# Kernel optimization log

Measured on AMD Instinct MI355X. Metric: run time of the kernel, lower is better.

Reference implementation:

```python
import math
import jax, jax.numpy as jnp
import numpy as np

D_MODEL = 1024
D_FF = 4096
NUM_EXPERTS = 8
TOP_K = 2
CAP_FACTOR = 1.0
AUX_COEF = 0.01
Z_COEF = 0.0


def setup_inputs() -> dict:
    key = jax.random.key(0)
    ks = jax.random.split(key, 6)
    x = jax.random.normal(ks[0], (4, 2048, D_MODEL), dtype=jnp.float32)
    router_w = jax.random.normal(ks[1], (D_MODEL, NUM_EXPERTS), dtype=jnp.float32) / math.sqrt(D_MODEL)
    router_b = jnp.zeros((NUM_EXPERTS,), dtype=jnp.float32)
    w1 = jax.random.normal(ks[2], (NUM_EXPERTS, D_MODEL, D_FF), dtype=jnp.float32) / math.sqrt(D_MODEL)
    w3 = jax.random.normal(ks[3], (NUM_EXPERTS, D_MODEL, D_FF), dtype=jnp.float32) / math.sqrt(D_MODEL)
    w2 = jax.random.normal(ks[4], (NUM_EXPERTS, D_FF, D_MODEL), dtype=jnp.float32) / math.sqrt(D_FF)
    return {"x": x, "router_w": router_w, "router_b": router_b, "w1": w1, "w3": w3, "w2": w2}


def reference(x, router_w, router_b, w1, w3, w2):
    b, s, d = x.shape
    E, k = NUM_EXPERTS, TOP_K
    T = b * s
    x_flat = x.reshape(T, d)

    # ---- router ----
    logits = x_flat @ router_w + router_b                      # [T, E]
    logits_f32 = logits.astype(jnp.float32)
    probs = jax.nn.softmax(logits_f32, axis=-1)                # [T, E]
    topk_p, topk_i = jax.lax.top_k(probs, k)                   # [T, k]
    topk_p = topk_p / jnp.clip(topk_p.sum(-1, keepdims=True), 1e-9)  # normalize_gates
    gate = topk_p.reshape(-1)                                  # [T*k]
    expert_idx = topk_i.reshape(-1)                            # [T*k]

    # ---- aux loss (load balance + z-loss) ----
    importance = probs.mean(axis=0)                            # [E]
    load = jnp.bincount(topk_i[:, 0], length=E).astype(jnp.float32) / T
    lb_loss = (importance * load).sum() * float(E)
    z_loss = jnp.mean(jnp.square(jax.nn.logsumexp(logits_f32, axis=-1)))
    aux_loss = (AUX_COEF * lb_loss + Z_COEF * z_loss).astype(x.dtype)

    # ---- capacity-based dispatch ----
    N = T * k
    cap = max(1, int(math.ceil(CAP_FACTOR * N / E)))
    x_rep = jnp.repeat(x_flat, k, axis=0)                      # [N, d]
    order = jnp.argsort(expert_idx)                            # stable sort by expert
    e_sorted = expert_idx[order]
    x_sorted = x_rep[order]
    g_sorted = gate[order].astype(x.dtype)
    counts = jnp.bincount(e_sorted, length=E)
    starts = jnp.concatenate([jnp.zeros((1,), counts.dtype), jnp.cumsum(counts)[:-1]])
    pos = jnp.arange(N, dtype=counts.dtype) - starts[e_sorted]   # rank within expert group
    keep = pos < cap
    slot = jnp.where(keep, e_sorted * cap + pos, E * cap)      # dropped tokens -> dump row

    buf = jnp.zeros((E * cap + 1, d), dtype=x.dtype).at[slot].set(x_sorted)
    buf = buf[: E * cap].reshape(E, cap, d)                    # [E, C, d]

    # ---- grouped SwiGLU experts ----
    h = jax.nn.silu(jnp.einsum('ecd,edf->ecf', buf, w1)) * jnp.einsum('ecd,edf->ecf', buf, w3)
    y = jnp.einsum('ecf,efd->ecd', h, w2).reshape(E * cap, d)

    # ---- combine ----
    gathered = y[jnp.minimum(slot, E * cap - 1)]
    out_sorted = jnp.where(keep[:, None], gathered, 0.0) * g_sorted[:, None]
    inv = jnp.argsort(order)
    out = out_sorted[inv].reshape(T, k, d).sum(axis=1)
    return out.reshape(b, s, d), aux_loss
```

## Files before the change

kernel.cpp:

```cpp
#include <hip/hip_runtime.h>
#include <hip/hip_bf16.h>
#include <math.h>

constexpr int kT    = 8192;
constexpr int kD    = 1024;
constexpr int kF    = 4096;
constexpr int kE    = 8;
constexpr int kN    = kT * 2;
constexpr int kCap  = 2048;
constexpr int kECap = kE * kCap;

typedef __attribute__((ext_vector_type(8))) short bf16x8;
typedef __attribute__((ext_vector_type(4))) float f32x4;

__device__ __forceinline__ void gload16(const __hip_bfloat16* g, __hip_bfloat16* l) {
  auto gp = (const __attribute__((address_space(1))) __hip_bfloat16*)g;
  auto lp = (__attribute__((address_space(3))) __hip_bfloat16*)l;
  __builtin_amdgcn_global_load_lds((const __attribute__((address_space(1))) void*)gp,
                                   (__attribute__((address_space(3))) void*)lp,
                                   16, 0, 0);
}

#define SYNC_VM(N) do { __builtin_amdgcn_sched_barrier(0); \
  asm volatile("s_waitcnt vmcnt(" #N ")" ::: "memory"); \
  __builtin_amdgcn_s_barrier(); \
  asm volatile("" ::: "memory"); } while (0)

__global__ void init_kernel(int* token_of) {
  int i = blockIdx.x * 256 + threadIdx.x;
  if (i < kECap) token_of[i] = -1;
}

__global__ __launch_bounds__(256)
void transpose_kernel(const float* __restrict__ src, __hip_bfloat16* __restrict__ dst,
                      int R, int C) {
  __shared__ float tile[32][33];
  const size_t mat = (size_t)R * C;
  const float* s = src + (size_t)blockIdx.z * mat;
  __hip_bfloat16* d = dst + (size_t)blockIdx.z * mat;
  int c0 = blockIdx.x * 32, r0 = blockIdx.y * 32;
  int tx = threadIdx.x, ty = threadIdx.y;
#pragma unroll
  for (int i = 0; i < 32; i += 8)
    tile[ty + i][tx] = s[(size_t)(r0 + ty + i) * C + (c0 + tx)];
  __syncthreads();
#pragma unroll
  for (int i = 0; i < 32; i += 8)
    d[(size_t)(c0 + ty + i) * R + (r0 + tx)] = __float2bfloat16(tile[tx][ty + i]);
}

__global__ __launch_bounds__(256)
void router_kernel(const float* __restrict__ x, const float* __restrict__ rw,
                   const float* __restrict__ rb, int* __restrict__ e_idx,
                   float* __restrict__ gates, float* __restrict__ probs_out) {
  int t = blockIdx.x * 4 + (threadIdx.x >> 6);
  int lane = threadIdx.x & 63;
  const float* xr = x + (size_t)t * kD;
  float acc[8];
#pragma unroll
  for (int e = 0; e < 8; ++e) acc[e] = 0.f;
  for (int i = 0; i < kD / 64; ++i) {
    int dd = i * 64 + lane;
    float xv = xr[dd];
    const float4* w4 = (const float4*)(rw + (size_t)dd * 8);
    float4 wa = w4[0], wb = w4[1];
    acc[0] += xv * wa.x; acc[1] += xv * wa.y; acc[2] += xv * wa.z; acc[3] += xv * wa.w;
    acc[4] += xv * wb.x; acc[5] += xv * wb.y; acc[6] += xv * wb.z; acc[7] += xv * wb.w;
  }
#pragma unroll
  for (int off = 32; off >= 1; off >>= 1) {
#pragma unroll
    for (int e = 0; e < 8; ++e) acc[e] += __shfl_xor(acc[e], off);
  }
  if (lane == 0) {
    float l[8], m = -1e30f;
#pragma unroll
    for (int e = 0; e < 8; ++e) { l[e] = acc[e] + rb[e]; m = fmaxf(m, l[e]); }
    float p[8], s = 0.f;
#pragma unroll
    for (int e = 0; e < 8; ++e) { p[e] = __expf(l[e] - m); s += p[e]; }
    float inv = 1.f / s;
#pragma unroll
    for (int e = 0; e < 8; ++e) p[e] *= inv;
    int i1 = 0;
#pragma unroll
    for (int e = 1; e < 8; ++e) if (p[e] > p[i1]) i1 = e;
    int i2 = (i1 == 0) ? 1 : 0;
#pragma unroll
    for (int e = 0; e < 8; ++e) if (e != i1 && e != i2 && p[e] > p[i2]) i2 = e;
    float den = fmaxf(p[i1] + p[i2], 1e-9f);
    e_idx[2 * t] = i1; e_idx[2 * t + 1] = i2;
    gates[2 * t] = p[i1] / den; gates[2 * t + 1] = p[i2] / den;
    float4* po = (float4*)(probs_out + (size_t)t * 8);
    po[0] = make_float4(p[0], p[1], p[2], p[3]);
    po[1] = make_float4(p[4], p[5], p[6], p[7]);
  }
}

__global__ __launch_bounds__(1024)
void aux_kernel(const float* __restrict__ probs, const int* __restrict__ e_idx,
                float* __restrict__ aux_out) {
  int tid = threadIdx.x, lane = tid & 63, wave = tid >> 6;
  float imp[8];
  int cnt[8];
#pragma unroll
  for (int e = 0; e < 8; ++e) { imp[e] = 0.f; cnt[e] = 0; }
  for (int t = tid; t < kT; t += 1024) {
    const float4* p4 = (const float4*)(probs + (size_t)t * 8);
    float4 a = p4[0], b = p4[1];
    imp[0] += a.x; imp[1] += a.y; imp[2] += a.z; imp[3] += a.w;
    imp[4] += b.x; imp[5] += b.y; imp[6] += b.z; imp[7] += b.w;
    ++cnt[e_idx[2 * t] & 7];
  }
#pragma unroll
  for (int off = 32; off >= 1; off >>= 1) {
#pragma unroll
    for (int e = 0; e < 8; ++e) {
      imp[e] += __shfl_xor(imp[e], off);
      cnt[e] += __shfl_xor(cnt[e], off);
    }
  }
  __shared__ float simp[16][8];
  __shared__ int scnt[16][8];
  if (lane == 0) {
#pragma unroll
    for (int e = 0; e < 8; ++e) { simp[wave][e] = imp[e]; scnt[wave][e] = cnt[e]; }
  }
  __syncthreads();
  if (tid == 0) {
    float lb = 0.f;
    for (int e = 0; e < 8; ++e) {
      float I = 0.f; int C = 0;
      for (int w = 0; w < 16; ++w) { I += simp[w][e]; C += scnt[w][e]; }
      lb += (I / (float)kT) * ((float)C / (float)kT);
    }
    aux_out[0] = 0.01f * lb * (float)kE;
  }
}

__global__ __launch_bounds__(256)
void rank_kernel(const int* __restrict__ e_idx, int* __restrict__ pos) {
  int e = blockIdx.x;
  __shared__ int wave_sum[4];
  __shared__ int running;
  int tid = threadIdx.x, lane = tid & 63, wave = tid >> 6;
  if (tid == 0) running = 0;
  __syncthreads();
  for (int base = 0; base < kN; base += 256) {
    int i = base + tid;
    bool f = (e_idx[i] == e);
    unsigned long long m = __ballot(f);
    int wpre = __popcll(m & ((1ull << lane) - 1ull));
    if (lane == 0) wave_sum[wave] = __popcll(m);
    __syncthreads();
    int woff = 0;
    for (int w = 0; w < wave; ++w) woff += wave_sum[w];
    int r = running;
    if (f) pos[i] = r + woff + wpre;
    __syncthreads();
    if (tid == 0) running = r + wave_sum[0] + wave_sum[1] + wave_sum[2] + wave_sum[3];
    __syncthreads();
  }
}

__global__ __launch_bounds__(256)
void scatter_kernel(const int* __restrict__ e_idx, const int* __restrict__ pos,
                    int* __restrict__ slot_of, int* __restrict__ token_of) {
  int i = blockIdx.x * 256 + threadIdx.x;
  if (i >= kN) return;
  int p = pos[i];
  if (p < kCap) {
    int slot = e_idx[i] * kCap + p;
    slot_of[i] = slot;
    token_of[slot] = i >> 1;
  } else {
    slot_of[i] = -1;
  }
}

struct __attribute__((aligned(8))) bf16x4s { __hip_bfloat16 v[4]; };

__global__ __launch_bounds__(64)
void gather_kernel(const float* __restrict__ x, const int* __restrict__ token_of,
                   __hip_bfloat16* __restrict__ buf) {
  int slot = blockIdx.x, lane = threadIdx.x;
  int t = token_of[slot];
  __hip_bfloat16* br = buf + (size_t)slot * kD;
  if (t >= 0) {
    const float* xr = x + (size_t)t * kD;
#pragma unroll
    for (int j = 0; j < 4; ++j) {
      int dd = (j * 64 + lane) * 4;
      float4 v = *(const float4*)(xr + dd);
      bf16x4s o;
      o.v[0] = __float2bfloat16(v.x); o.v[1] = __float2bfloat16(v.y);
      o.v[2] = __float2bfloat16(v.z); o.v[3] = __float2bfloat16(v.w);
      *(bf16x4s*)(br + dd) = o;
    }
  } else {
    bf16x4s z;
    z.v[0] = z.v[1] = z.v[2] = z.v[3] = __float2bfloat16(0.f);
#pragma unroll
    for (int j = 0; j < 4; ++j) *(bf16x4s*)(br + (j * 64 + lane) * 4) = z;
  }
}

__global__ __launch_bounds__(512, 2)
void gemm1_kernel(const __hip_bfloat16* __restrict__ Abase,
                  const __hip_bfloat16* __restrict__ W1t,
                  const __hip_bfloat16* __restrict__ W3t,
                  __hip_bfloat16* __restrict__ H) {
  constexpr int K = kD;
  constexpr int NT = K / 64;
  const int e = blockIdx.z, mt = blockIdx.y, ft = blockIdx.x;
  const int tid = threadIdx.x, lane = tid & 63, wave = tid >> 6;
  const int wr = wave >> 1, wc = wave & 1;
  const int frow = lane & 15, fk = lane >> 4;

  const __hip_bfloat16* A  = Abase + (size_t)(e * kCap + mt * 256) * K;
  const __hip_bfloat16* B1 = W1t + ((size_t)e * kF + ft * 128) * K;
  const __hip_bfloat16* B3 = W3t + ((size_t)e * kF + ft * 128) * K;

  extern __shared__ __hip_bfloat16 lds[];

  f32x4 accU[4][4], accV[4][4];
#pragma unroll
  for (int m = 0; m < 4; ++m)
#pragma unroll
    for (int n = 0; n < 4; ++n) {
      accU[m][n] = (f32x4){0.f, 0.f, 0.f, 0.f};
      accV[m][n] = (f32x4){0.f, 0.f, 0.f, 0.f};
    }

  auto stageA = [&](int t, int b) {
#pragma unroll
    for (int j = 0; j < 4; ++j) {
      int c = j * 128 + wc * 64 + lane;
      int rl = c >> 3, s = c & 7;
      const __hip_bfloat16* g = A + (size_t)(wr * 64 + rl) * K + t * 64 + (s ^ (rl & 7)) * 8;
      gload16(g, &lds[b * 32768 + wr * 4096 + (j * 128 + wc * 64) * 8]);
    }
  };
  auto stageB1 = [&](int t, int b) {
#pragma unroll
    for (int j = 0; j < 2; ++j) {
      int c = j * 256 + wr * 64 + lane;
      int rl = c >> 3, s = c & 7;
      const __hip_bfloat16* g = B1 + (size_t)(wc * 64 + rl) * K + t * 64 + (s ^ (rl & 7)) * 8;
      gload16(g, &lds[b * 32768 + 16384 + wc * 4096 + (j * 256 + wr * 64) * 8]);
    }
  };
  auto stageB3 = [&](int t, int b) {
#pragma unroll
    for (int j = 0; j < 2; ++j) {
      int c = j * 256 + wr * 64 + lane;
      int rl = c >> 3, s = c & 7;
      const __hip_bfloat16* g = B3 + (size_t)(wc * 64 + rl) * K + t * 64 + (s ^ (rl & 7)) * 8;
      gload16(g, &lds[b * 32768 + 16384 + 8192 + wc * 4096 + (j * 256 + wr * 64) * 8]);
    }
  };
  auto phase = [&](int b, f32x4 (&ac)[4][4], bf16x8 (&af)[4][2], int broff, bool loadA) {
    if (loadA) {
#pragma unroll
      for (int m = 0; m < 4; ++m)
#pragma unroll
        for (int h = 0; h < 2; ++h) {
          int row = wr * 64 + m * 16 + frow;
          af[m][h] = *(const bf16x8*)&lds[b * 32768 + row * 64 + ((h * 4 + fk) ^ (row & 7)) * 8];
        }
    }
    bf16x8 bf[4][2];
#pragma unroll
    for (int n = 0; n < 4; ++n)
#pragma unroll
      for (int h = 0; h < 2; ++h) {
        int row = broff + wc * 64 + n * 16 + frow;
        bf[n][h] = *(const bf16x8*)&lds[b * 32768 + 16384 + row * 64 + ((h * 4 + fk) ^ (row & 7)) * 8];
      }
    __builtin_amdgcn_s_setprio(1);
#pragma unroll
    for (int m = 0; m < 4; ++m)
#pragma unroll
      for (int n = 0; n < 4; ++n)
#pragma unroll
        for (int h = 0; h < 2; ++h)
          ac[m][n] = __builtin_amdgcn_mfma_f32_16x16x32_bf16(af[m][h], bf[n][h], ac[m][n], 0, 0, 0);
    __builtin_amdgcn_s_setprio(0);
    __builtin_amdgcn_sched_barrier(0);
  };

  stageA(0, 0); stageB1(0, 0); stageB3(0, 0);

  for (int t = 0; t < NT; ++t) {
    const int b = t & 1, nb = b ^ 1;
    const bool nx = (t + 1 < NT);
    SYNC_VM(2);
    if (nx) stageA(t + 1, nb);
    bf16x8 af[4][2];
    phase(b, accU, af, 0, true);
    if (nx) { SYNC_VM(4); } else { SYNC_VM(0); }
    if (nx) stageB1(t + 1, nb);
    phase(b, accV, af, 128, false);
    if (nx) stageB3(t + 1, nb);
  }

  __hip_bfloat16* Ht = H + (size_t)(e * kCap + mt * 256) * kF + ft * 128;
#pragma unroll
  for (int m = 0; m < 4; ++m)
#pragma unroll
    for (int n = 0; n < 4; ++n)
#pragma unroll
      for (int r = 0; r < 4; ++r) {
        int row = wr * 64 + m * 16 + fk * 4 + r;
        int col = wc * 64 + n * 16 + frow;
        float u = accU[m][n][r], v = accV[m][n][r];
        float hval = (u / (1.f + __expf(-u))) * v;
        Ht[(size_t)row * kF + col] = __float2bfloat16(hval);
      }
}

__global__ __launch_bounds__(512, 2)
void gemm2_kernel(const __hip_bfloat16* __restrict__ Hbase,
                  const __hip_bfloat16* __restrict__ W2t,
                  float* __restrict__ Y) {
  constexpr int K = kF;
  constexpr int NT = K / 64;
  const int e = blockIdx.z, mt = blockIdx.y, nt = blockIdx.x;
  const int tid = threadIdx.x, lane = tid & 63, wave = tid >> 6;
  const int wr = wave >> 2, wc = wave & 3;
  const int frow = lane & 15, fk = lane >> 4;

  const __hip_bfloat16* A = Hbase + (size_t)(e * kCap + mt * 256) * K;
  const __hip_bfloat16* B = W2t + ((size_t)e * kD + nt * 256) * K;

  extern __shared__ __hip_bfloat16 lds[];

  f32x4 acc[2][4][4];
#pragma unroll
  for (int p = 0; p < 2; ++p)
#pragma unroll
    for (int m = 0; m < 4; ++m)
#pragma unroll
      for (int n = 0; n < 4; ++n) acc[p][m][n] = (f32x4){0.f, 0.f, 0.f, 0.f};

  auto stageB = [&](int t, int b) {
#pragma unroll
    for (int j = 0; j < 4; ++j) {
      int c = j * 128 + wr * 64 + lane;
      int rl = c >> 3, s = c & 7;
      const __hip_bfloat16* g = B + (size_t)(wc * 64 + rl) * K + t * 64 + (s ^ (rl & 7)) * 8;
      gload16(g, &lds[b * 32768 + 16384 + wc * 4096 + (j * 128 + wr * 64) * 8]);
    }
  };
  auto stageA = [&](int t, int p, int b) {
    int q = 2 * wr + p;
#pragma unroll
    for (int j = 0; j < 2; ++j) {
      int c = j * 256 + wc * 64 + lane;
      int rl = c >> 3, s = c & 7;
      const __hip_bfloat16* g = A + (size_t)(q * 64 + rl) * K + t * 64 + (s ^ (rl & 7)) * 8;
      gload16(g, &lds[b * 32768 + q * 4096 + (j * 256 + wc * 64) * 8]);
    }
  };
  auto phase = [&](int b, int p, f32x4 (&ac)[4][4], bf16x8 (&bf)[4][2], bool loadB) {
    bf16x8 a[4][2];
#pragma unroll
    for (int m = 0; m < 4; ++m)
#pragma unroll
      for (int h = 0; h < 2; ++h) {
        int row = wr * 128 + p * 64 + m * 16 + frow;
        a[m][h] = *(const bf16x8*)&lds[b * 32768 + row * 64 + ((h * 4 + fk) ^ (row & 7)) * 8];
      }
    if (loadB) {
#pragma unroll
      for (int n = 0; n < 4; ++n)
#pragma unroll
        for (int h = 0; h < 2; ++h) {
          int row = wc * 64 + n * 16 + frow;
          bf[n][h] = *(const bf16x8*)&lds[b * 32768 + 16384 + row * 64 + ((h * 4 + fk) ^ (row & 7)) * 8];
        }
    }
    __builtin_amdgcn_s_setprio(1);
#pragma unroll
    for (int m = 0; m < 4; ++m)
#pragma unroll
      for (int n = 0; n < 4; ++n)
#pragma unroll
        for (int h = 0; h < 2; ++h)
          ac[m][n] = __builtin_amdgcn_mfma_f32_16x16x32_bf16(a[m][h], bf[n][h], ac[m][n], 0, 0, 0);
    __builtin_amdgcn_s_setprio(0);
    __builtin_amdgcn_sched_barrier(0);
  };

  stageB(0, 0); stageA(0, 0, 0); stageA(0, 1, 0);

  for (int t = 0; t < NT; ++t) {
    const int b = t & 1, nb = b ^ 1;
    const bool nx = (t + 1 < NT);
    SYNC_VM(2);
    if (nx) stageB(t + 1, nb);
    bf16x8 bf[4][2];
    phase(b, 0, acc[0], bf, true);
    if (nx) { SYNC_VM(4); } else { SYNC_VM(0); }
    if (nx) stageA(t + 1, 0, nb);
    phase(b, 1, acc[1], bf, false);
    if (nx) stageA(t + 1, 1, nb);
  }

  float* Yt = Y + (size_t)(e * kCap + mt * 256) * kD + nt * 256;
#pragma unroll
  for (int p = 0; p < 2; ++p)
#pragma unroll
    for (int m = 0; m < 4; ++m)
#pragma unroll
      for (int n = 0; n < 4; ++n)
#pragma unroll
        for (int r = 0; r < 4; ++r) {
          int row = wr * 128 + p * 64 + m * 16 + fk * 4 + r;
          int col = wc * 64 + n * 16 + frow;
          Yt[(size_t)row * kD + col] = acc[p][m][n][r];
        }
}

__global__ __launch_bounds__(256)
void combine_kernel(const float* __restrict__ Y, const int* __restrict__ slot_of,
                    const float* __restrict__ gates, float* __restrict__ out) {
  int t = blockIdx.x;
  int dd = threadIdx.x * 4;
  int s0 = slot_of[2 * t], s1 = slot_of[2 * t + 1];
  float g0 = gates[2 * t], g1 = gates[2 * t + 1];
  float4 r = {0.f, 0.f, 0.f, 0.f};
  if (s0 >= 0) {
    float4 v = *(const float4*)(Y + (size_t)s0 * kD + dd);
    r.x += g0 * v.x; r.y += g0 * v.y; r.z += g0 * v.z; r.w += g0 * v.w;
  }
  if (s1 >= 0) {
    float4 v = *(const float4*)(Y + (size_t)s1 * kD + dd);
    r.x += g1 * v.x; r.y += g1 * v.y; r.z += g1 * v.z; r.w += g1 * v.w;
  }
  *(float4*)(out + (size_t)t * kD + dd) = r;
}

extern "C" void kernel_launch(void* const* d_in, const int* in_sizes, int n_in,
                              void* d_out, int out_size, void* d_ws, size_t ws_size,
                              hipStream_t stream) {
  (void)in_sizes; (void)n_in; (void)out_size; (void)ws_size;
  const float* x  = (const float*)d_in[0];
  const float* rw = (const float*)d_in[1];
  const float* rb = (const float*)d_in[2];
  const float* w1 = (const float*)d_in[3];
  const float* w3 = (const float*)d_in[4];
  const float* w2 = (const float*)d_in[5];
  float* out = (float*)d_out;

  char* base = (char*)d_ws;
  size_t off = 0;
  auto alloc = [&](size_t bytes) -> char* {
    char* r = base + off;
    off += (bytes + 255) & ~(size_t)255;
    return r;
  };
  __hip_bfloat16* w1t = (__hip_bfloat16*)alloc((size_t)kE * kF * kD * 2);
  __hip_bfloat16* w3t = (__hip_bfloat16*)alloc((size_t)kE * kF * kD * 2);
  __hip_bfloat16* w2t = (__hip_bfloat16*)alloc((size_t)kE * kD * kF * 2);
  __hip_bfloat16* buf = (__hip_bfloat16*)alloc((size_t)kECap * kD * 2);
  __hip_bfloat16* h   = (__hip_bfloat16*)alloc((size_t)kECap * kF * 2);
  float*          y   = (float*)alloc((size_t)kECap * kD * 4);
  int*   e_idx    = (int*)alloc((size_t)kN * 4);
  float* gates    = (float*)alloc((size_t)kN * 4);
  int*   pos      = (int*)alloc((size_t)kN * 4);
  int*   slot_of  = (int*)alloc((size_t)kN * 4);
  int*   token_of = (int*)alloc((size_t)kECap * 4);
  float* probs    = (float*)alloc((size_t)kT * 8 * 4);

  init_kernel<<<kECap / 256, 256, 0, stream>>>(token_of);
  transpose_kernel<<<dim3(kF / 32, kD / 32, kE), dim3(32, 8, 1), 0, stream>>>(w1, w1t, kD, kF);
  transpose_kernel<<<dim3(kF / 32, kD / 32, kE), dim3(32, 8, 1), 0, stream>>>(w3, w3t, kD, kF);
  transpose_kernel<<<dim3(kD / 32, kF / 32, kE), dim3(32, 8, 1), 0, stream>>>(w2, w2t, kF, kD);
  router_kernel<<<kT / 4, 256, 0, stream>>>(x, rw, rb, e_idx, gates, probs);
  aux_kernel<<<1, 1024, 0, stream>>>(probs, e_idx, out + (size_t)kT * kD);
  rank_kernel<<<kE, 256, 0, stream>>>(e_idx, pos);
  scatter_kernel<<<kN / 256, 256, 0, stream>>>(e_idx, pos, slot_of, token_of);
  gather_kernel<<<kECap, 64, 0, stream>>>(x, token_of, buf);
  gemm1_kernel<<<dim3(kF / 128, kCap / 256, kE), 512, 131072, stream>>>(buf, w1t, w3t, h);
  gemm2_kernel<<<dim3(kD / 256, kCap / 256, kE), 512, 131072, stream>>>(h, w2t, y);
  combine_kernel<<<kT, 256, 0, stream>>>(y, slot_of, gates, out);
}
```

Before: 608.2 us.

## Restructure expert GEMMs into 8-phase ping-pong pipeline with finer-grained staging

```diff
diff --git a/kernel.cpp b/kernel.cpp
--- a/kernel.cpp
+++ b/kernel.cpp
@@ -21,10 +21,16 @@
                                    16, 0, 0);
 }
 
-#define SYNC_VM(N) do { __builtin_amdgcn_sched_barrier(0); \
-  asm volatile("s_waitcnt vmcnt(" #N ")" ::: "memory"); \
+#define BAR_ENTER() do { __builtin_amdgcn_sched_barrier(0); \
   __builtin_amdgcn_s_barrier(); \
-  asm volatile("" ::: "memory"); } while (0)
+  asm volatile("s_waitcnt lgkmcnt(0)" ::: "memory"); \
+  __builtin_amdgcn_sched_barrier(0); \
+  __builtin_amdgcn_s_setprio(1); } while (0)
+#define BAR_EXIT() do { __builtin_amdgcn_s_setprio(0); \
+  __builtin_amdgcn_sched_barrier(0); \
+  __builtin_amdgcn_s_barrier(); \
+  __builtin_amdgcn_sched_barrier(0); } while (0)
+#define WAIT_VM(N) asm volatile("s_waitcnt vmcnt(" #N ")" ::: "memory")
 
 __global__ void init_kernel(int* token_of) {
   int i = blockIdx.x * 256 + threadIdx.x;
@@ -212,6 +218,7 @@
                   __hip_bfloat16* __restrict__ H) {
   constexpr int K = kD;
   constexpr int NT = K / 64;
+  constexpr int NI = NT / 2;
   const int e = blockIdx.z, mt = blockIdx.y, ft = blockIdx.x;
   const int tid = threadIdx.x, lane = tid & 63, wave = tid >> 6;
   const int wr = wave >> 1, wc = wave & 1;
@@ -232,76 +239,79 @@
       accV[m][n] = (f32x4){0.f, 0.f, 0.f, 0.f};
     }
 
-  auto stageA = [&](int t, int b) {
-#pragma unroll
-    for (int j = 0; j < 4; ++j) {
-      int c = j * 128 + wc * 64 + lane;
+  auto stg = [&](const __hip_bfloat16* gbase, int rowbase, int t, int ldsbase) {
+#pragma unroll
+    for (int j = 0; j < 2; ++j) {
+      int c = j * 512 + tid;
       int rl = c >> 3, s = c & 7;
-      const __hip_bfloat16* g = A + (size_t)(wr * 64 + rl) * K + t * 64 + (s ^ (rl & 7)) * 8;
-      gload16(g, &lds[b * 32768 + wr * 4096 + (j * 128 + wc * 64) * 8]);
-    }
-  };
-  auto stageB1 = [&](int t, int b) {
-#pragma unroll
-    for (int j = 0; j < 2; ++j) {
-      int c = j * 256 + wr * 64 + lane;
-      int rl = c >> 3, s = c & 7;
-      const __hip_bfloat16* g = B1 + (size_t)(wc * 64 + rl) * K + t * 64 + (s ^ (rl & 7)) * 8;
-      gload16(g, &lds[b * 32768 + 16384 + wc * 4096 + (j * 256 + wr * 64) * 8]);
-    }
-  };
-  auto stageB3 = [&](int t, int b) {
-#pragma unroll
-    for (int j = 0; j < 2; ++j) {
-      int c = j * 256 + wr * 64 + lane;
-      int rl = c >> 3, s = c & 7;
-      const __hip_bfloat16* g = B3 + (size_t)(wc * 64 + rl) * K + t * 64 + (s ^ (rl & 7)) * 8;
-      gload16(g, &lds[b * 32768 + 16384 + 8192 + wc * 4096 + (j * 256 + wr * 64) * 8]);
-    }
-  };
-  auto phase = [&](int b, f32x4 (&ac)[4][4], bf16x8 (&af)[4][2], int broff, bool loadA) {
-    if (loadA) {
-#pragma unroll
-      for (int m = 0; m < 4; ++m)
-#pragma unroll
-        for (int h = 0; h < 2; ++h) {
-          int row = wr * 64 + m * 16 + frow;
-          af[m][h] = *(const bf16x8*)&lds[b * 32768 + row * 64 + ((h * 4 + fk) ^ (row & 7)) * 8];
-        }
-    }
-    bf16x8 bf[4][2];
-#pragma unroll
-    for (int n = 0; n < 4; ++n)
-#pragma unroll
-      for (int h = 0; h < 2; ++h) {
-        int row = broff + wc * 64 + n * 16 + frow;
-        bf[n][h] = *(const bf16x8*)&lds[b * 32768 + 16384 + row * 64 + ((h * 4 + fk) ^ (row & 7)) * 8];
-      }
-    __builtin_amdgcn_s_setprio(1);
+      const __hip_bfloat16* g = gbase + (size_t)(rowbase + rl) * K + t * 64 + (s ^ (rl & 7)) * 8;
+      gload16(g, &lds[ldsbase + (j * 512 + wave * 64) * 8]);
+    }
+  };
+  auto rdA = [&](int b, int h, bf16x8 (&a)[4][2]) {
+#pragma unroll
+    for (int m = 0; m < 4; ++m) {
+      int row = wr * 64 + m * 16 + frow;
+      a[m][h] = *(const bf16x8*)&lds[b * 32768 + row * 64 + ((h * 4 + fk) ^ (row & 7)) * 8];
+    }
+  };
+  auto rdB = [&](int b, int roff, int h, bf16x8 (&bb)[4]) {
+#pragma unroll
+    for (int n = 0; n < 4; ++n) {
+      int row = roff + wc * 64 + n * 16 + frow;
+      bb[n] = *(const bf16x8*)&lds[b * 32768 + 16384 + row * 64 + ((h * 4 + fk) ^ (row & 7)) * 8];
+    }
+  };
+  auto mm16 = [&](bf16x8 (&a)[4][2], int h, bf16x8 (&bb)[4], f32x4 (&ac)[4][4]) {
 #pragma unroll
     for (int m = 0; m < 4; ++m)
 #pragma unroll
       for (int n = 0; n < 4; ++n)
-#pragma unroll
-        for (int h = 0; h < 2; ++h)
-          ac[m][n] = __builtin_amdgcn_mfma_f32_16x16x32_bf16(af[m][h], bf[n][h], ac[m][n], 0, 0, 0);
+        ac[m][n] = __builtin_amdgcn_mfma_f32_16x16x32_bf16(a[m][h], bb[n], ac[m][n], 0, 0, 0);
+  };
+
+  stg(A, 0, 0, 0);
+  stg(A, 128, 0, 8192);
+  stg(B1, 0, 0, 16384);
+  stg(B3, 0, 0, 24576);
+  stg(A, 0, 1, 32768);
+  stg(A, 128, 1, 32768 + 8192);
+  WAIT_VM(4);
+  __builtin_amdgcn_s_barrier();
+  __builtin_amdgcn_sched_barrier(0);
+
+  for (int i = 0; i < NI; ++i) {
+    const int v = 2 * i + 1, u2 = 2 * i + 2, v2 = 2 * i + 3;
+    const bool more = (i + 1 < NI);
+    bf16x8 a[4][2], bb[4];
+    rdA(0, 0, a); rdB(0, 0, 0, bb);
+    stg(B3, 0, v, 32768 + 24576);
+    BAR_ENTER(); mm16(a, 0, bb, accU); BAR_EXIT();
+    rdA(0, 1, a); rdB(0, 0, 1, bb);
+    stg(B1, 0, v, 32768 + 16384);
+    BAR_ENTER(); mm16(a, 1, bb, accU); BAR_EXIT();
+    rdB(0, 128, 0, bb);
+    if (more) stg(A, 0, u2, 0);
+    BAR_ENTER(); mm16(a, 0, bb, accV); BAR_EXIT();
+    rdB(0, 128, 1, bb);
+    if (more) { stg(A, 128, u2, 8192); WAIT_VM(4); }
+    else      { WAIT_VM(0); }
+    BAR_ENTER(); mm16(a, 1, bb, accV); BAR_EXIT();
+    rdA(1, 0, a); rdB(1, 0, 0, bb);
+    if (more) stg(B1, 0, u2, 16384);
+    BAR_ENTER(); mm16(a, 0, bb, accU); BAR_EXIT();
+    rdA(1, 1, a); rdB(1, 0, 1, bb);
+    if (more) stg(B3, 0, u2, 24576);
+    BAR_ENTER(); mm16(a, 1, bb, accU); BAR_EXIT();
+    rdB(1, 128, 0, bb);
+    if (more) stg(A, 0, v2, 32768);
+    BAR_ENTER(); mm16(a, 0, bb, accV); BAR_EXIT();
+    rdB(1, 128, 1, bb);
+    if (more) { stg(A, 128, v2, 32768 + 8192); WAIT_VM(4); }
+    BAR_ENTER(); mm16(a, 1, bb, accV);
     __builtin_amdgcn_s_setprio(0);
     __builtin_amdgcn_sched_barrier(0);
-  };
-
-  stageA(0, 0); stageB1(0, 0); stageB3(0, 0);
-
-  for (int t = 0; t < NT; ++t) {
-    const int b = t & 1, nb = b ^ 1;
-    const bool nx = (t + 1 < NT);
-    SYNC_VM(2);
-    if (nx) stageA(t + 1, nb);
-    bf16x8 af[4][2];
-    phase(b, accU, af, 0, true);
-    if (nx) { SYNC_VM(4); } else { SYNC_VM(0); }
-    if (nx) stageB1(t + 1, nb);
-    phase(b, accV, af, 128, false);
-    if (nx) stageB3(t + 1, nb);
+    if (more) { __builtin_amdgcn_s_barrier(); __builtin_amdgcn_sched_barrier(0); }
   }
 
   __hip_bfloat16* Ht = H + (size_t)(e * kCap + mt * 256) * kF + ft * 128;
@@ -325,6 +335,7 @@
                   float* __restrict__ Y) {
   constexpr int K = kF;
   constexpr int NT = K / 64;
+  constexpr int NI = NT / 2;
   const int e = blockIdx.z, mt = blockIdx.y, nt = blockIdx.x;
   const int tid = threadIdx.x, lane = tid & 63, wave = tid >> 6;
   const int wr = wave >> 2, wc = wave & 3;
@@ -335,91 +346,103 @@
 
   extern __shared__ __hip_bfloat16 lds[];
 
-  f32x4 acc[2][4][4];
-#pragma unroll
-  for (int p = 0; p < 2; ++p)
+  f32x4 acc[8][4];
+#pragma unroll
+  for (int m = 0; m < 8; ++m)
+#pragma unroll
+    for (int n = 0; n < 4; ++n) acc[m][n] = (f32x4){0.f, 0.f, 0.f, 0.f};
+
+  auto stg = [&](const __hip_bfloat16* gbase, int rowbase, int t, int ldsbase) {
+#pragma unroll
+    for (int j = 0; j < 2; ++j) {
+      int c = j * 512 + tid;
+      int rl = c >> 3, s = c & 7;
+      const __hip_bfloat16* g = gbase + (size_t)(rowbase + rl) * K + t * 64 + (s ^ (rl & 7)) * 8;
+      gload16(g, &lds[ldsbase + (j * 512 + wave * 64) * 8]);
+    }
+  };
+  auto rdA = [&](int b, int mh, bf16x8 (&af)[4][2]) {
 #pragma unroll
     for (int m = 0; m < 4; ++m)
 #pragma unroll
-      for (int n = 0; n < 4; ++n) acc[p][m][n] = (f32x4){0.f, 0.f, 0.f, 0.f};
-
-  auto stageB = [&](int t, int b) {
-#pragma unroll
-    for (int j = 0; j < 4; ++j) {
-      int c = j * 128 + wr * 64 + lane;
-      int rl = c >> 3, s = c & 7;
-      const __hip_bfloat16* g = B + (size_t)(wc * 64 + rl) * K + t * 64 + (s ^ (rl & 7)) * 8;
-      gload16(g, &lds[b * 32768 + 16384 + wc * 4096 + (j * 128 + wr * 64) * 8]);
-    }
-  };
-  auto stageA = [&](int t, int p, int b) {
-    int q = 2 * wr + p;
-#pragma unroll
-    for (int j = 0; j < 2; ++j) {
-      int c = j * 256 + wc * 64 + lane;
-      int rl = c >> 3, s = c & 7;
-      const __hip_bfloat16* g = A + (size_t)(q * 64 + rl) * K + t * 64 + (s ^ (rl & 7)) * 8;
-      gload16(g, &lds[b * 32768 + q * 4096 + (j * 256 + wc * 64) * 8]);
-    }
-  };
-  auto phase = [&](int b, int p, f32x4 (&ac)[4][4], bf16x8 (&bf)[4][2], bool loadB) {
-    bf16x8 a[4][2];
+      for (int h = 0; h < 2; ++h) {
+        int row = wr * 128 + mh * 64 + m * 16 + frow;
+        af[m][h] = *(const bf16x8*)&lds[b * 32768 + row * 64 + ((h * 4 + fk) ^ (row & 7)) * 8];
+      }
+  };
+  auto rdB = [&](int b, int nh, bf16x8 (&bf)[2][2]) {
+#pragma unroll
+    for (int n = 0; n < 2; ++n)
+#pragma unroll
+      for (int h = 0; h < 2; ++h) {
+        int row = wc * 64 + nh * 32 + n * 16 + frow;
+        bf[n][h] = *(const bf16x8*)&lds[b * 32768 + 16384 + row * 64 + ((h * 4 + fk) ^ (row & 7)) * 8];
+      }
+  };
+  auto mm16 = [&](bf16x8 (&af)[4][2], bf16x8 (&bf)[2][2], int mh, int nh) {
 #pragma unroll
     for (int m = 0; m < 4; ++m)
 #pragma unroll
-      for (int h = 0; h < 2; ++h) {
-        int row = wr * 128 + p * 64 + m * 16 + frow;
-        a[m][h] = *(const bf16x8*)&lds[b * 32768 + row * 64 + ((h * 4 + fk) ^ (row & 7)) * 8];
-      }
-    if (loadB) {
-#pragma unroll
-      for (int n = 0; n < 4; ++n)
-#pragma unroll
-        for (int h = 0; h < 2; ++h) {
-          int row = wc * 64 + n * 16 + frow;
-          bf[n][h] = *(const bf16x8*)&lds[b * 32768 + 16384 + row * 64 + ((h * 4 + fk) ^ (row & 7)) * 8];
-        }
-    }
-    __builtin_amdgcn_s_setprio(1);
-#pragma unroll
-    for (int m = 0; m < 4; ++m)
-#pragma unroll
-      for (int n = 0; n < 4; ++n)
+      for (int n = 0; n < 2; ++n)
 #pragma unroll
         for (int h = 0; h < 2; ++h)
-          ac[m][n] = __builtin_amdgcn_mfma_f32_16x16x32_bf16(a[m][h], bf[n][h], ac[m][n], 0, 0, 0);
+          acc[mh * 4 + m][nh * 2 + n] = __builtin_amdgcn_mfma_f32_16x16x32_bf16(
+              af[m][h], bf[n][h], acc[mh * 4 + m][nh * 2 + n], 0, 0, 0);
+  };
+
+  stg(B, 0, 0, 16384);
+  stg(B, 128, 0, 24576);
+  stg(A, 0, 0, 0);
+  stg(A, 128, 0, 8192);
+  stg(B, 0, 1, 32768 + 16384);
+  stg(B, 128, 1, 32768 + 24576);
+  WAIT_VM(4);
+  __builtin_amdgcn_s_barrier();
+  __builtin_amdgcn_sched_barrier(0);
+
+  for (int i = 0; i < NI; ++i) {
+    const int v = 2 * i + 1, u2 = 2 * i + 2, v2 = 2 * i + 3;
+    const bool more = (i + 1 < NI);
+    bf16x8 af[4][2], bf0[2][2], bf1[2][2];
+    rdA(0, 0, af); rdB(0, 0, bf0);
+    stg(A, 0, v, 32768);
+    BAR_ENTER(); mm16(af, bf0, 0, 0); BAR_EXIT();
+    rdB(0, 1, bf1);
+    stg(A, 128, v, 32768 + 8192);
+    BAR_ENTER(); mm16(af, bf1, 0, 1); BAR_EXIT();
+    rdA(0, 1, af);
+    if (more) stg(B, 0, u2, 16384);
+    BAR_ENTER(); mm16(af, bf0, 1, 0); BAR_EXIT();
+    if (more) { stg(B, 128, u2, 24576); WAIT_VM(4); }
+    else      { WAIT_VM(0); }
+    BAR_ENTER(); mm16(af, bf1, 1, 1); BAR_EXIT();
+    rdA(1, 0, af); rdB(1, 0, bf0);
+    if (more) stg(A, 0, u2, 0);
+    BAR_ENTER(); mm16(af, bf0, 0, 0); BAR_EXIT();
+    rdB(1, 1, bf1);
+    if (more) stg(A, 128, u2, 8192);
+    BAR_ENTER(); mm16(af, bf1, 0, 1); BAR_EXIT();
+    rdA(1, 1, af);
+    if (more) stg(B, 0, v2, 32768 + 16384);
+    BAR_ENTER(); mm16(af, bf0, 1, 0); BAR_EXIT();
+    if (more) { stg(B, 128, v2, 32768 + 24576); WAIT_VM(4); }
+    BAR_ENTER(); mm16(af, bf1, 1, 1);
     __builtin_amdgcn_s_setprio(0);
     __builtin_amdgcn_sched_barrier(0);
-  };
-
-  stageB(0, 0); stageA(0, 0, 0); stageA(0, 1, 0);
-
-  for (int t = 0; t < NT; ++t) {
-    const int b = t & 1, nb = b ^ 1;
-    const bool nx = (t + 1 < NT);
-    SYNC_VM(2);
-    if (nx) stageB(t + 1, nb);
-    bf16x8 bf[4][2];
-    phase(b, 0, acc[0], bf, true);
-    if (nx) { SYNC_VM(4); } else { SYNC_VM(0); }
-    if (nx) stageA(t + 1, 0, nb);
-    phase(b, 1, acc[1], bf, false);
-    if (nx) stageA(t + 1, 1, nb);
+    if (more) { __builtin_amdgcn_s_barrier(); __builtin_amdgcn_sched_barrier(0); }
   }
 
   float* Yt = Y + (size_t)(e * kCap + mt * 256) * kD + nt * 256;
 #pragma unroll
-  for (int p = 0; p < 2; ++p)
-#pragma unroll
-    for (int m = 0; m < 4; ++m)
-#pragma unroll
-      for (int n = 0; n < 4; ++n)
-#pragma unroll
-        for (int r = 0; r < 4; ++r) {
-          int row = wr * 128 + p * 64 + m * 16 + fk * 4 + r;
-          int col = wc * 64 + n * 16 + frow;
-          Yt[(size_t)row * kD + col] = acc[p][m][n][r];
-        }
+  for (int m = 0; m < 8; ++m)
+#pragma unroll
+    for (int n = 0; n < 4; ++n)
+#pragma unroll
+      for (int r = 0; r < 4; ++r) {
+        int row = wr * 128 + m * 16 + fk * 4 + r;
+        int col = wc * 64 + n * 16 + frow;
+        Yt[(size_t)row * kD + col] = acc[m][n][r];
+      }
 }
 
 __global__ __launch_bounds__(256)
```

New measurement: 754.3 us. 24.0% more time.
